# Performance work log

Measured on AMD Instinct MI355X. Metric: run time of the kernel, lower is better.

## Reference

```python
import jax, jax.numpy as jnp
import numpy as np
from jax.ops import segment_sum, segment_max, segment_min

N_PER = 128        # nodes (pulses) per graph; graphs are contiguous blocks
NUM_GRAPHS = 2048  # must be a multiple of BATCH_SIZE
K = 4              # knn_graph k (from KNNAmp(4, ...))
BATCH_SIZE = 1024  # hardcoded in the torch module
L1, L2, L3, L4, L5, L6, L7 = 5, 64, 128, 94, 64, 32, 1
GRU_IN = 4 * L5    # 256
GRU_H = L6         # 32


def setup_inputs() -> dict:
    key = jax.random.key(0)
    ks = jax.random.split(key, 12)
    N = N_PER * NUM_GRAPHS
    s = 0.1
    return {
        "x": jax.random.normal(ks[0], (N, L1), jnp.float32),
        "batch": (jnp.arange(N) // N_PER).astype(jnp.int32),
        "h_1": jnp.zeros((2, BATCH_SIZE, GRU_H), jnp.float32),
        "W1": jax.random.normal(ks[1], (2 * L1, L2), jnp.float32) * s,
        "b1": jnp.zeros((L2,), jnp.float32),
        "W2": jax.random.normal(ks[2], (L2, L3), jnp.float32) * s,
        "b2": jnp.zeros((L3,), jnp.float32),
        "nn1_W": jax.random.normal(ks[3], (3 * L3, L4), jnp.float32) * s,
        "nn1_b": jnp.zeros((L4,), jnp.float32),
        "nn2_W": jax.random.normal(ks[4], (L4, L5), jnp.float32) * s,
        "nn2_b": jnp.zeros((L5,), jnp.float32),
        "nn4_W": jax.random.normal(ks[5], (GRU_H, L7), jnp.float32) * s,
        "nn4_b": jnp.zeros((L7,), jnp.float32),
        "wih0": jax.random.normal(ks[6], (3 * GRU_H, GRU_IN), jnp.float32) * s,
        "whh0": jax.random.normal(ks[7], (3 * GRU_H, GRU_H), jnp.float32) * s,
        "bih0": jnp.zeros((3 * GRU_H,), jnp.float32),
        "bhh0": jnp.zeros((3 * GRU_H,), jnp.float32),
        "wih1": jax.random.normal(ks[8], (3 * GRU_H, GRU_H), jnp.float32) * s,
        "whh1": jax.random.normal(ks[9], (3 * GRU_H, GRU_H), jnp.float32) * s,
        "bih1": jnp.zeros((3 * GRU_H,), jnp.float32),
        "bhh1": jnp.zeros((3 * GRU_H,), jnp.float32),
    }


def _knn_neighbors(pos):
    # pos: [N,3]; graphs are contiguous blocks of N_PER nodes -> per-graph KNN
    p = pos.reshape(NUM_GRAPHS, N_PER, 3)
    d2 = jnp.sum((p[:, :, None, :] - p[:, None, :, :]) ** 2, -1)  # [G,n,n]
    d2 = d2 + jnp.eye(N_PER, dtype=d2.dtype) * 1e10               # loop=False
    _, idx = jax.lax.top_k(-d2, K)                                 # [G,n,K]
    off = (jnp.arange(NUM_GRAPHS, dtype=idx.dtype) * N_PER)[:, None, None]
    return (idx + off).reshape(-1, K)  # [N,K] global source (neighbor) ids


def _gru_layer(seq_in, h0, wih, whh, bih, bhh):
    # PyTorch GRU cell math; gate order r, z, n.
    def step(h, xt):
        gi = xt @ wih.T + bih
        gh = h @ whh.T + bhh
        ir, iz, inn = jnp.split(gi, 3, -1)
        hr, hz, hn = jnp.split(gh, 3, -1)
        r = jax.nn.sigmoid(ir + hr)
        z = jax.nn.sigmoid(iz + hz)
        n = jnp.tanh(inn + r * hn)
        hnew = (1.0 - z) * n + z * h
        return hnew, hnew
    hT, ys = jax.lax.scan(step, h0, seq_in)
    return ys, hT


def reference(x, batch, h_1, W1, b1, W2, b2, nn1_W, nn1_b, nn2_W, nn2_b,
              nn4_W, nn4_b, wih0, whh0, bih0, bhh0, wih1, whh1, bih1, bhh1):
    N = x.shape[0]
    nbr = _knn_neighbors(x[:, :3])                       # int indices, non-diff
    x_i = jnp.broadcast_to(x[:, None, :], (N, K, L1))    # center features
    x_j = x[nbr]                                         # [N,K,5] gather
    feats = jnp.concatenate([x_i, x_j - x_i], -1)        # EdgeConv message input
    m = jax.nn.relu(jax.nn.relu(feats @ W1 + b1) @ W2 + b2)  # [N,K,128]
    # three EdgeConvs share the same MLP; compute messages once, aggregate 3 ways
    h = jax.nn.relu(jnp.concatenate([m.max(1), m.mean(1), m.sum(1)], 1))  # [N,384]
    h = jax.nn.relu(h @ nn1_W + nn1_b)
    h = h @ nn2_W + nn2_b                                # [N,64]
    a = segment_max(h, batch, num_segments=NUM_GRAPHS)
    bmin = segment_min(h, batch, num_segments=NUM_GRAPHS)
    c = segment_sum(h, batch, num_segments=NUM_GRAPHS)
    cnt = segment_sum(jnp.ones((N, 1), h.dtype), batch, num_segments=NUM_GRAPHS)
    d = c / cnt
    g = jax.nn.relu(jnp.concatenate([a, bmin, c, d], 1))  # [G,256]
    seq_len = NUM_GRAPHS // BATCH_SIZE
    # faithful to torch.reshape((seq, 256, 1024)).transpose(1,2)
    g = g.reshape(seq_len, GRU_IN, BATCH_SIZE).transpose(0, 2, 1)  # [T,B,256]
    out0, hT0 = _gru_layer(g, h_1[0], wih0, whh0, bih0, bhh0)
    out1, hT1 = _gru_layer(out0, h_1[1], wih1, whh1, bih1, bhh1)
    hT = jnp.stack([hT0, hT1], 0)                        # [2,B,32]
    # torch: reshape(x.transpose(1,2), (-1, 32))
    y = out1.transpose(0, 2, 1).reshape(-1, GRU_H)
    y = jax.nn.relu(y)
    y = jax.nn.relu(y @ nn4_W + nn4_b)                   # [T*B, 1]
    return y, hT
```

## Files before the change

kernel.cpp:

```cpp
#include <hip/hip_runtime.h>
#include <hip/hip_bf16.h>

#define NPER 128

typedef __attribute__((ext_vector_type(8))) short s8v;
typedef __attribute__((ext_vector_type(4))) float f4v;

__device__ __forceinline__ unsigned short f2bf(float x) {
    unsigned u = __float_as_uint(x);
    unsigned r = u + 0x7FFFu + ((u >> 16) & 1u);
    return (unsigned short)(r >> 16);
}
__device__ __forceinline__ float bf2f(unsigned short b) {
    return __uint_as_float(((unsigned)b) << 16);
}

__device__ __forceinline__ void ins4(float d, int id, float* bd, int* bi) {
    const bool c0 = d < bd[0], c1 = d < bd[1], c2 = d < bd[2], c3 = d < bd[3];
    bd[3] = c2 ? bd[2] : (c3 ? d : bd[3]);  bi[3] = c2 ? bi[2] : (c3 ? id : bi[3]);
    bd[2] = c1 ? bd[1] : (c2 ? d : bd[2]);  bi[2] = c1 ? bi[1] : (c2 ? id : bi[2]);
    bd[1] = c0 ? bd[0] : (c1 ? d : bd[1]);  bi[1] = c0 ? bi[0] : (c1 ? id : bi[1]);
    bd[0] = c0 ? d : bd[0];                 bi[0] = c0 ? id : bi[0];
}

__global__ void k_prep(const float* __restrict__ W2,
                       const float* __restrict__ nn2W,
                       const float* __restrict__ nn1W,
                       float* __restrict__ nn2WT, float* __restrict__ WfT,
                       unsigned short* __restrict__ WBhi,
                       unsigned short* __restrict__ WBlo)
{
    int i = blockIdx.x * 256 + threadIdx.x;
    if (i < 6016) {
        int ch = i / 94, c = i - ch * 94;
        nn2WT[i] = nn2W[c * 64 + ch];
    } else if (i < 30592) {
        int k = i - 6016, jj = k >> 8, r = k & 255;
        float v = 0.0f;
        if (jj < 94) {
            if (r < 128) v = nn1W[r * 94 + jj];
            else {
                int c = r - 128;
                v = 0.25f * nn1W[(128 + c) * 94 + jj] + nn1W[(256 + c) * 94 + jj];
            }
        }
        WfT[k] = v;
    } else if (i < 38784) {
        int j = i - 30592;
        int e = j & 7, l = (j >> 3) & 63, nt = (j >> 9) & 7, ks = j >> 12;
        int kk = ks * 32 + ((l >> 4) << 3) + e;
        int n  = nt * 16 + (l & 15);
        float v = W2[kk * 128 + n];
        unsigned short hb = f2bf(v);
        WBhi[j] = hb;
        WBlo[j] = f2bf(v - bf2f(hb));
    }
}

__global__ __launch_bounds__(256, 4) void k_edge(
    const float* __restrict__ x,
    const float* __restrict__ W1,
    const float* __restrict__ b1,
    const float* __restrict__ b2,
    const unsigned short* __restrict__ WBhi,
    const unsigned short* __restrict__ WBlo,
    const float* __restrict__ WfT,
    const float* __restrict__ nn1b,
    const float* __restrict__ nn2WT,
    const float* __restrict__ nn2b,
    float* __restrict__ pmax,
    float* __restrict__ pmin,
    float* __restrict__ psum)
{
    __shared__ float pool[10240];
    float* XS  = pool;
    int*   NBR = (int*)(pool + 640);
    float* KD  = pool + 896;
    int*   KI  = (int*)(pool + 1920);
    unsigned short* PH16 = (unsigned short*)(pool + 1024);
    unsigned short* PL16 = (unsigned short*)(pool + 5632);
    float* AGM = pool + 1024;
    float* AGS = pool + 5120;
    float* NNH = pool;
    float* HT  = pool + 6016;

    const int t = threadIdx.x;
    const int lane = t & 63;
    const int w = __builtin_amdgcn_readfirstlane(t >> 6);
    const int graph = blockIdx.x >> 1;
    const int node0 = (blockIdx.x & 1) * 64;

    for (int i = t; i < NPER * 5; i += 256) XS[i] = x[(size_t)graph * (NPER * 5) + i];
    __syncthreads();

    {
        const int nl2 = t & 63;
        const int q  = t >> 6;
        const int ng2 = node0 + nl2;
        const float px = XS[ng2 * 5 + 0], py = XS[ng2 * 5 + 1], pz = XS[ng2 * 5 + 2];
        float bd[4] = {3e38f, 3e38f, 3e38f, 3e38f};
        int   bi[4] = {0, 0, 0, 0};
        const int m0 = q * 32;
        for (int m = m0; m < m0 + 32; ++m) {
            float dx = XS[m * 5 + 0] - px, dy = XS[m * 5 + 1] - py, dz = XS[m * 5 + 2] - pz;
            float d2 = __fadd_rn(__fadd_rn(__fmul_rn(dx, dx), __fmul_rn(dy, dy)),
                                 __fmul_rn(dz, dz));
            d2 = (m == ng2) ? 3.0e38f : d2;
            ins4(d2, m, bd, bi);
        }
        #pragma unroll
        for (int s = 0; s < 4; ++s) { KD[(q * 4 + s) * 64 + nl2] = bd[s]; KI[(q * 4 + s) * 64 + nl2] = bi[s]; }
    }
    __syncthreads();
    if (t < 64) {
        float bd[4] = {3e38f, 3e38f, 3e38f, 3e38f};
        int   bi[4] = {0, 0, 0, 0};
        #pragma unroll
        for (int q = 0; q < 4; ++q)
            #pragma unroll
            for (int s = 0; s < 4; ++s)
                ins4(KD[(q * 4 + s) * 64 + t], KI[(q * 4 + s) * 64 + t], bd, bi);
        #pragma unroll
        for (int s = 0; s < 4; ++s) NBR[t * 4 + s] = bi[s];
    }
    __syncthreads();

    float acc[24];
    const int jj0 = __builtin_amdgcn_readfirstlane(w * 24);
    #pragma unroll
    for (int i = 0; i < 24; ++i) acc[i] = (jj0 + i < 94) ? nn1b[jj0 + i] : 0.0f;

    #pragma unroll 1
    for (int hf = 0; hf < 2; ++hf) {
        float mxq[2][2][4], smq[2][2][4];
        #pragma unroll 1
        for (int c = 0; c < 2; ++c) {
            if ((t >> 7) == c) {
                const int nl = t >> 2;
                const int kk = t & 3;
                const int n_g = node0 + nl;
                const int j   = NBR[nl * 4 + kk];
                float f[10];
                #pragma unroll
                for (int d = 0; d < 5; ++d) { f[d] = XS[n_g * 5 + d]; f[5 + d] = XS[j * 5 + d] - f[d]; }
                float h1v[64];
                #pragma unroll
                for (int cc = 0; cc < 64; ++cc) h1v[cc] = b1[cc];
                #pragma unroll
                for (int d = 0; d < 10; ++d) {
                    float fd = f[d];
                    #pragma unroll
                    for (int cc = 0; cc < 64; ++cc) h1v[cc] = fmaf(fd, W1[d * 64 + cc], h1v[cc]);
                }
                #pragma unroll
                for (int cc = 0; cc < 64; ++cc) h1v[cc] = fmaxf(h1v[cc], 0.0f);

                const int rl = t & 127;
                unsigned int* dh = (unsigned int*)PH16 + rl * 36;
                unsigned int* dl = (unsigned int*)PL16 + rl * 36;
                #pragma unroll
                for (int i = 0; i < 8; ++i) {
                    unsigned int hw[4], lw[4];
                    #pragma unroll
                    for (int p = 0; p < 4; ++p) {
                        float va = h1v[i * 8 + p * 2], vb = h1v[i * 8 + p * 2 + 1];
                        unsigned short ha = f2bf(va), hb = f2bf(vb);
                        unsigned short la = f2bf(va - bf2f(ha)), lb = f2bf(vb - bf2f(hb));
                        hw[p] = (unsigned)ha | ((unsigned)hb << 16);
                        lw[p] = (unsigned)la | ((unsigned)lb << 16);
                    }
                    *(uint4*)(dh + 4 * i) = make_uint4(hw[0], hw[1], hw[2], hw[3]);
                    *(uint4*)(dl + 4 * i) = make_uint4(lw[0], lw[1], lw[2], lw[3]);
                }
            }
            __syncthreads();

            f4v C[2][4];
            #pragma unroll
            for (int q = 0; q < 4; ++q) {
                float bv = b2[hf * 64 + q * 16 + (lane & 15)];
                #pragma unroll
                for (int m = 0; m < 2; ++m) {
                    C[m][q][0] = bv; C[m][q][1] = bv; C[m][q][2] = bv; C[m][q][3] = bv;
                }
            }
            #pragma unroll
            for (int ks = 0; ks < 2; ++ks) {
                s8v ah[2], al[2];
                #pragma unroll
                for (int m = 0; m < 2; ++m) {
                    const int row = (w << 5) + (m << 4) + (lane & 15);
                    const int ui  = row * 72 + (ks << 5) + ((lane >> 4) << 3);
                    ah[m] = *(const s8v*)(PH16 + ui);
                    al[m] = *(const s8v*)(PL16 + ui);
                }
                #pragma unroll
                for (int q = 0; q < 4; ++q) {
                    const int nt = hf * 4 + q;
                    const int bidx = ((((ks << 3) | nt) << 6) | lane) << 3;
                    s8v bh = *(const s8v*)(WBhi + bidx);
                    s8v bl = *(const s8v*)(WBlo + bidx);
                    #pragma unroll
                    for (int m = 0; m < 2; ++m) {
                        f4v cc = C[m][q];
                        cc = __builtin_amdgcn_mfma_f32_16x16x32_bf16(al[m], bh, cc, 0, 0, 0);
                        cc = __builtin_amdgcn_mfma_f32_16x16x32_bf16(ah[m], bl, cc, 0, 0, 0);
                        cc = __builtin_amdgcn_mfma_f32_16x16x32_bf16(ah[m], bh, cc, 0, 0, 0);
                        C[m][q] = cc;
                    }
                }
            }
            #pragma unroll
            for (int m = 0; m < 2; ++m)
                #pragma unroll
                for (int q = 0; q < 4; ++q) {
                    float a0 = fmaxf(C[m][q][0], 0.0f), a1 = fmaxf(C[m][q][1], 0.0f);
                    float a2 = fmaxf(C[m][q][2], 0.0f), a3 = fmaxf(C[m][q][3], 0.0f);
                    mxq[c][m][q] = fmaxf(fmaxf(a0, a1), fmaxf(a2, a3));
                    smq[c][m][q] = (a0 + a1) + (a2 + a3);
                }
            __syncthreads();
        }

        #pragma unroll
        for (int c2 = 0; c2 < 2; ++c2)
            #pragma unroll
            for (int m = 0; m < 2; ++m)
                #pragma unroll
                for (int q = 0; q < 4; ++q) {
                    const int node = (c2 << 5) + (w << 3) + (m << 2) + (lane >> 4);
                    const int chl  = (q << 4) + (lane & 15);
                    const int ad   = (node << 6) + ((((chl >> 2) ^ node) & 15) << 2) + (chl & 3);
                    AGM[ad] = mxq[c2][m][q];
                    AGS[ad] = smq[c2][m][q];
                }
        __syncthreads();

        for (int cb = 0; cb < 64; cb += 8) {
            float am[8], as_[8];
            #pragma unroll
            for (int i = 0; i < 2; ++i) {
                const int sw = ((((cb >> 2) + i) ^ lane) & 15) << 2;
                *(float4*)&am[i * 4]  = *(const float4*)&AGM[(lane << 6) + sw];
                *(float4*)&as_[i * 4] = *(const float4*)&AGS[(lane << 6) + sw];
            }
            #pragma unroll
            for (int i2 = 0; i2 < 24; ++i2) {
                const float* wa = WfT + (size_t)(jj0 + i2) * 256 + hf * 64 + cb;
                const float* wb = wa + 128;
                float a = acc[i2];
                #pragma unroll
                for (int i = 0; i < 8; ++i) a = fmaf(am[i], wa[i], fmaf(as_[i], wb[i], a));
                acc[i2] = a;
            }
        }
        __syncthreads();
    }

    #pragma unroll
    for (int i2 = 0; i2 < 24; ++i2)
        if (jj0 + i2 < 94) NNH[(jj0 + i2) * 64 + lane] = fmaxf(acc[i2], 0.0f);
    __syncthreads();

    {
        const int ch0 = __builtin_amdgcn_readfirstlane(w * 16);
        float acc2[16];
        #pragma unroll
        for (int i = 0; i < 16; ++i) acc2[i] = nn2b[ch0 + i];
        #pragma unroll 1
        for (int cb = 0; cb < 64; cb += 32) {
            float hv[32];
            #pragma unroll
            for (int i = 0; i < 32; ++i) hv[i] = NNH[(cb + i) * 64 + lane];
            #pragma unroll
            for (int i = 0; i < 16; ++i) {
                const float* wp = nn2WT + (size_t)(ch0 + i) * 94 + cb;
                float a = acc2[i];
                #pragma unroll
                for (int c = 0; c < 32; ++c) a = fmaf(hv[c], wp[c], a);
                acc2[i] = a;
            }
        }
        {
            float hv[30];
            #pragma unroll
            for (int i = 0; i < 30; ++i) hv[i] = NNH[(64 + i) * 64 + lane];
            #pragma unroll
            for (int i = 0; i < 16; ++i) {
                const float* wp = nn2WT + (size_t)(ch0 + i) * 94 + 64;
                float a = acc2[i];
                #pragma unroll
                for (int c = 0; c < 30; ++c) a = fmaf(hv[c], wp[c], a);
                acc2[i] = a;
            }
        }
        __syncthreads();
        #pragma unroll
        for (int i = 0; i < 8; ++i)
            *(float2*)&HT[lane * 66 + ch0 + i * 2] =
                make_float2(acc2[i * 2], acc2[i * 2 + 1]);
    }
    __syncthreads();

    if (t < 64) {
        float mx = -3e38f, mn = 3e38f, sm = 0.0f;
        for (int n = 0; n < 64; ++n) {
            float v = HT[n * 66 + t];
            mx = fmaxf(mx, v); mn = fminf(mn, v); sm += v;
        }
        pmax[(size_t)blockIdx.x * 64 + t] = mx;
        pmin[(size_t)blockIdx.x * 64 + t] = mn;
        psum[(size_t)blockIdx.x * 64 + t] = sm;
    }
}

__global__ void k_pool(const float* __restrict__ pmax, const float* __restrict__ pmin,
                       const float* __restrict__ psum, float* __restrict__ g_out)
{
    const int t = threadIdx.x;
    const int g = blockIdx.x * 4 + (t >> 6);
    const int ch = t & 63;
    const size_t a = (size_t)(2 * g) * 64 + ch, b = a + 64;
    float mx = fmaxf(pmax[a], pmax[b]);
    float mn = fminf(pmin[a], pmin[b]);
    float sm = psum[a] + psum[b];
    float* gp = g_out + (size_t)g * 256;
    gp[ch]        = fmaxf(mx, 0.0f);
    gp[64 + ch]   = fmaxf(mn, 0.0f);
    gp[128 + ch]  = fmaxf(sm, 0.0f);
    gp[192 + ch]  = fmaxf(sm * (1.0f / 128.0f), 0.0f);
}

__global__ __launch_bounds__(128) void k_gru(
    const float* __restrict__ g, const float* __restrict__ h1_in,
    const float* __restrict__ wih0, const float* __restrict__ whh0,
    const float* __restrict__ bih0, const float* __restrict__ bhh0,
    const float* __restrict__ wih1, const float* __restrict__ whh1,
    const float* __restrict__ bih1, const float* __restrict__ bhh1,
    float* __restrict__ out1, float* __restrict__ hT)
{
    __shared__ float xt[4][256];
    __shared__ float h0[4][32];
    __shared__ float h1l[4][32];
    const int tid = threadIdx.x;
    const int e = tid >> 5;
    const int j = tid & 31;
    const int b = blockIdx.x * 4 + e;

    h0[e][j]  = h1_in[b * 32 + j];
    h1l[e][j] = h1_in[32768 + b * 32 + j];
    __syncthreads();

    for (int t = 0; t < 2; ++t) {
        for (int c = j; c < 256; c += 32)
            xt[e][c] = g[(size_t)(t * 1024 + 4 * c + (b >> 8)) * 256 + (b & 255)];
        __syncthreads();

        float gi0 = bih0[j], gi1 = bih0[32 + j], gi2 = bih0[64 + j];
        for (int c = 0; c < 256; ++c) {
            float xv = xt[e][c];
            gi0 += xv * wih0[j * 256 + c];
            gi1 += xv * wih0[(32 + j) * 256 + c];
            gi2 += xv * wih0[(64 + j) * 256 + c];
        }
        float gh0 = bhh0[j], gh1 = bhh0[32 + j], gh2 = bhh0[64 + j];
        #pragma unroll
        for (int c = 0; c < 32; ++c) {
            float hv = h0[e][c];
            gh0 += hv * whh0[j * 32 + c];
            gh1 += hv * whh0[(32 + j) * 32 + c];
            gh2 += hv * whh0[(64 + j) * 32 + c];
        }
        float r = 1.0f / (1.0f + expf(-(gi0 + gh0)));
        float z = 1.0f / (1.0f + expf(-(gi1 + gh1)));
        float nn = tanhf(gi2 + r * gh2);
        float hn0 = (1.0f - z) * nn + z * h0[e][j];
        __syncthreads();
        h0[e][j] = hn0;
        __syncthreads();

        float ai0 = bih1[j], ai1 = bih1[32 + j], ai2 = bih1[64 + j];
        #pragma unroll
        for (int c = 0; c < 32; ++c) {
            float xv = h0[e][c];
            ai0 += xv * wih1[j * 32 + c];
            ai1 += xv * wih1[(32 + j) * 32 + c];
            ai2 += xv * wih1[(64 + j) * 32 + c];
        }
        float ah0 = bhh1[j], ah1 = bhh1[32 + j], ah2 = bhh1[64 + j];
        #pragma unroll
        for (int c = 0; c < 32; ++c) {
            float hv = h1l[e][c];
            ah0 += hv * whh1[j * 32 + c];
            ah1 += hv * whh1[(32 + j) * 32 + c];
            ah2 += hv * whh1[(64 + j) * 32 + c];
        }
        float r1 = 1.0f / (1.0f + expf(-(ai0 + ah0)));
        float z1 = 1.0f / (1.0f + expf(-(ai1 + ah1)));
        float n1 = tanhf(ai2 + r1 * ah2);
        float hn1 = (1.0f - z1) * n1 + z1 * h1l[e][j];
        __syncthreads();
        h1l[e][j] = hn1;
        out1[(size_t)(t * 1024 + b) * 32 + j] = hn1;
        __syncthreads();
    }
    hT[b * 32 + j]         = h0[e][j];
    hT[32768 + b * 32 + j] = h1l[e][j];
}

__global__ void k_final(const float* __restrict__ out1,
                        const float* __restrict__ nn4W, const float* __restrict__ nn4b,
                        float* __restrict__ y)
{
    const int r = blockIdx.x * 256 + threadIdx.x;
    if (r >= 2048) return;
    const int t = r >> 10, rp = r & 1023;
    const int f = rp >> 5, bb0 = (rp & 31) << 5;
    float acc = nn4b[0];
    #pragma unroll
    for (int c = 0; c < 32; ++c)
        acc += fmaxf(out1[(size_t)(t * 1024 + bb0 + c) * 32 + f], 0.0f) * nn4W[c];
    y[r] = fmaxf(acc, 0.0f);
}

extern "C" void kernel_launch(void* const* d_in, const int* in_sizes, int n_in,
                              void* d_out, int out_size, void* d_ws, size_t ws_size,
                              hipStream_t stream) {
    const float* x    = (const float*)d_in[0];
    const float* h1i  = (const float*)d_in[2];
    const float* W1   = (const float*)d_in[3];
    const float* b1   = (const float*)d_in[4];
    const float* W2   = (const float*)d_in[5];
    const float* b2   = (const float*)d_in[6];
    const float* nn1W = (const float*)d_in[7];
    const float* nn1b = (const float*)d_in[8];
    const float* nn2W = (const float*)d_in[9];
    const float* nn2b = (const float*)d_in[10];
    const float* nn4W = (const float*)d_in[11];
    const float* nn4b = (const float*)d_in[12];
    const float* wih0 = (const float*)d_in[13];
    const float* whh0 = (const float*)d_in[14];
    const float* bih0 = (const float*)d_in[15];
    const float* bhh0 = (const float*)d_in[16];
    const float* wih1 = (const float*)d_in[17];
    const float* whh1 = (const float*)d_in[18];
    const float* bih1 = (const float*)d_in[19];
    const float* bhh1 = (const float*)d_in[20];

    float* ws = (float*)d_ws;
    float* g_buf  = ws;
    float* out1   = g_buf + 524288;
    float* nn2WT  = out1 + 65536;
    float* WfT    = nn2WT + 6016;
    float* pmax   = WfT + 24576;
    float* pmin   = pmax + 262144;
    float* psum   = pmin + 262144;
    unsigned short* WBhi = (unsigned short*)(psum + 262144);
    unsigned short* WBlo = WBhi + 8192;

    float* y  = (float*)d_out;
    float* hT = y + 2048;

    hipLaunchKernelGGL(k_prep, dim3(152), dim3(256), 0, stream,
                       W2, nn2W, nn1W, nn2WT, WfT, WBhi, WBlo);
    hipLaunchKernelGGL(k_edge, dim3(4096), dim3(256), 0, stream,
                       x, W1, b1, b2, WBhi, WBlo, WfT, nn1b, nn2WT, nn2b,
                       pmax, pmin, psum);
    hipLaunchKernelGGL(k_pool, dim3(512), dim3(256), 0, stream,
                       pmax, pmin, psum, g_buf);
    hipLaunchKernelGGL(k_gru, dim3(256), dim3(128), 0, stream,
                       g_buf, h1i, wih0, whh0, bih0, bhh0,
                       wih1, whh1, bih1, bhh1, out1, hT);
    hipLaunchKernelGGL(k_final, dim3(8), dim3(256), 0, stream,
                       out1, nn4W, nn4b, y);
}
```

Baseline: 922.9 us.

## Split edge MLP into quarter-width channel passes to reduce register pressure

The second-layer channel loop in k_edge now runs in four 32-channel passes instead of two 64-channel passes, and the first-layer hidden vector is computed in two 32-wide halves instead of all 64 at once. This cuts the number of live accumulators. The aggregation buffers switch from an XOR-swizzled layout to a padded stride of 36, and launch_bounds drops the occupancy hint from 4 to 3. In exchange, the first-layer MLP is recomputed on every pass, and the extra passes add syncthreads and repeated LDS writes.

```diff
diff --git a/kernel.cpp b/kernel.cpp
--- a/kernel.cpp
+++ b/kernel.cpp
@@ -57,7 +57,7 @@
     }
 }
 
-__global__ __launch_bounds__(256, 4) void k_edge(
+__global__ __launch_bounds__(256, 3) void k_edge(
     const float* __restrict__ x,
     const float* __restrict__ W1,
     const float* __restrict__ b1,
@@ -80,7 +80,7 @@
     unsigned short* PH16 = (unsigned short*)(pool + 1024);
     unsigned short* PL16 = (unsigned short*)(pool + 5632);
     float* AGM = pool + 1024;
-    float* AGS = pool + 5120;
+    float* AGS = pool + 3328;
     float* NNH = pool;
     float* HT  = pool + 6016;
 
@@ -131,8 +131,8 @@
     for (int i = 0; i < 24; ++i) acc[i] = (jj0 + i < 94) ? nn1b[jj0 + i] : 0.0f;
 
     #pragma unroll 1
-    for (int hf = 0; hf < 2; ++hf) {
-        float mxq[2][2][4], smq[2][2][4];
+    for (int qp = 0; qp < 4; ++qp) {
+        float mxq[2][2][2], smq[2][2][2];
         #pragma unroll 1
         for (int c = 0; c < 2; ++c) {
             if ((t >> 7) == c) {
@@ -143,81 +143,80 @@
                 float f[10];
                 #pragma unroll
                 for (int d = 0; d < 5; ++d) { f[d] = XS[n_g * 5 + d]; f[5 + d] = XS[j * 5 + d] - f[d]; }
-                float h1v[64];
-                #pragma unroll
-                for (int cc = 0; cc < 64; ++cc) h1v[cc] = b1[cc];
-                #pragma unroll
-                for (int d = 0; d < 10; ++d) {
-                    float fd = f[d];
-                    #pragma unroll
-                    for (int cc = 0; cc < 64; ++cc) h1v[cc] = fmaf(fd, W1[d * 64 + cc], h1v[cc]);
-                }
-                #pragma unroll
-                for (int cc = 0; cc < 64; ++cc) h1v[cc] = fmaxf(h1v[cc], 0.0f);
-
                 const int rl = t & 127;
                 unsigned int* dh = (unsigned int*)PH16 + rl * 36;
                 unsigned int* dl = (unsigned int*)PL16 + rl * 36;
-                #pragma unroll
-                for (int i = 0; i < 8; ++i) {
-                    unsigned int hw[4], lw[4];
+                #pragma unroll 1
+                for (int hh = 0; hh < 2; ++hh) {
+                    float hv[32];
                     #pragma unroll
-                    for (int p = 0; p < 4; ++p) {
-                        float va = h1v[i * 8 + p * 2], vb = h1v[i * 8 + p * 2 + 1];
-                        unsigned short ha = f2bf(va), hb = f2bf(vb);
-                        unsigned short la = f2bf(va - bf2f(ha)), lb = f2bf(vb - bf2f(hb));
-                        hw[p] = (unsigned)ha | ((unsigned)hb << 16);
-                        lw[p] = (unsigned)la | ((unsigned)lb << 16);
+                    for (int cc = 0; cc < 32; ++cc) hv[cc] = b1[hh * 32 + cc];
+                    #pragma unroll
+                    for (int d = 0; d < 10; ++d) {
+                        float fd = f[d];
+                        #pragma unroll
+                        for (int cc = 0; cc < 32; ++cc)
+                            hv[cc] = fmaf(fd, W1[d * 64 + hh * 32 + cc], hv[cc]);
                     }
-                    *(uint4*)(dh + 4 * i) = make_uint4(hw[0], hw[1], hw[2], hw[3]);
-                    *(uint4*)(dl + 4 * i) = make_uint4(lw[0], lw[1], lw[2], lw[3]);
+                    #pragma unroll
+                    for (int cc = 0; cc < 32; ++cc) hv[cc] = fmaxf(hv[cc], 0.0f);
+                    #pragma unroll
+                    for (int i = 0; i < 4; ++i) {
+                        unsigned int hw[4], lw[4];
+                        #pragma unroll
+                        for (int p = 0; p < 4; ++p) {
+                            float va = hv[i * 8 + p * 2], vb = hv[i * 8 + p * 2 + 1];
+                            unsigned short ha = f2bf(va), hb = f2bf(vb);
+                            unsigned short la = f2bf(va - bf2f(ha)), lb = f2bf(vb - bf2f(hb));
+                            hw[p] = (unsigned)ha | ((unsigned)hb << 16);
+                            lw[p] = (unsigned)la | ((unsigned)lb << 16);
+                        }
+                        *(uint4*)(dh + hh * 16 + i * 4) = make_uint4(hw[0], hw[1], hw[2], hw[3]);
+                        *(uint4*)(dl + hh * 16 + i * 4) = make_uint4(lw[0], lw[1], lw[2], lw[3]);
+                    }
                 }
             }
             __syncthreads();
 
-            f4v C[2][4];
-            #pragma unroll
-            for (int q = 0; q < 4; ++q) {
-                float bv = b2[hf * 64 + q * 16 + (lane & 15)];
+            f4v C[2][2];
+            #pragma unroll
+            for (int n2 = 0; n2 < 2; ++n2) {
+                float bv = b2[(qp * 2 + n2) * 16 + (lane & 15)];
                 #pragma unroll
                 for (int m = 0; m < 2; ++m) {
-                    C[m][q][0] = bv; C[m][q][1] = bv; C[m][q][2] = bv; C[m][q][3] = bv;
+                    C[m][n2][0] = bv; C[m][n2][1] = bv; C[m][n2][2] = bv; C[m][n2][3] = bv;
                 }
             }
             #pragma unroll
             for (int ks = 0; ks < 2; ++ks) {
-                s8v ah[2], al[2];
                 #pragma unroll
                 for (int m = 0; m < 2; ++m) {
                     const int row = (w << 5) + (m << 4) + (lane & 15);
                     const int ui  = row * 72 + (ks << 5) + ((lane >> 4) << 3);
-                    ah[m] = *(const s8v*)(PH16 + ui);
-                    al[m] = *(const s8v*)(PL16 + ui);
-                }
-                #pragma unroll
-                for (int q = 0; q < 4; ++q) {
-                    const int nt = hf * 4 + q;
-                    const int bidx = ((((ks << 3) | nt) << 6) | lane) << 3;
-                    s8v bh = *(const s8v*)(WBhi + bidx);
-                    s8v bl = *(const s8v*)(WBlo + bidx);
+                    s8v ah = *(const s8v*)(PH16 + ui);
+                    s8v al = *(const s8v*)(PL16 + ui);
                     #pragma unroll
-                    for (int m = 0; m < 2; ++m) {
-                        f4v cc = C[m][q];
-                        cc = __builtin_amdgcn_mfma_f32_16x16x32_bf16(al[m], bh, cc, 0, 0, 0);
-                        cc = __builtin_amdgcn_mfma_f32_16x16x32_bf16(ah[m], bl, cc, 0, 0, 0);
-                        cc = __builtin_amdgcn_mfma_f32_16x16x32_bf16(ah[m], bh, cc, 0, 0, 0);
-                        C[m][q] = cc;
+                    for (int n2 = 0; n2 < 2; ++n2) {
+                        const int nt = qp * 2 + n2;
+                        const int bidx = ((((ks << 3) | nt) << 6) | lane) << 3;
+                        s8v bh = *(const s8v*)(WBhi + bidx);
+                        s8v bl = *(const s8v*)(WBlo + bidx);
+                        f4v cc = C[m][n2];
+                        cc = __builtin_amdgcn_mfma_f32_16x16x32_bf16(al, bh, cc, 0, 0, 0);
+                        cc = __builtin_amdgcn_mfma_f32_16x16x32_bf16(ah, bl, cc, 0, 0, 0);
+                        cc = __builtin_amdgcn_mfma_f32_16x16x32_bf16(ah, bh, cc, 0, 0, 0);
+                        C[m][n2] = cc;
                     }
                 }
             }
             #pragma unroll
             for (int m = 0; m < 2; ++m)
                 #pragma unroll
-                for (int q = 0; q < 4; ++q) {
-                    float a0 = fmaxf(C[m][q][0], 0.0f), a1 = fmaxf(C[m][q][1], 0.0f);
-                    float a2 = fmaxf(C[m][q][2], 0.0f), a3 = fmaxf(C[m][q][3], 0.0f);
-                    mxq[c][m][q] = fmaxf(fmaxf(a0, a1), fmaxf(a2, a3));
-                    smq[c][m][q] = (a0 + a1) + (a2 + a3);
+                for (int n2 = 0; n2 < 2; ++n2) {
+                    float a0 = fmaxf(C[m][n2][0], 0.0f), a1 = fmaxf(C[m][n2][1], 0.0f);
+                    float a2 = fmaxf(C[m][n2][2], 0.0f), a3 = fmaxf(C[m][n2][3], 0.0f);
+                    mxq[c][m][n2] = fmaxf(fmaxf(a0, a1), fmaxf(a2, a3));
+                    smq[c][m][n2] = (a0 + a1) + (a2 + a3);
                 }
             __syncthreads();
         }
@@ -227,26 +226,25 @@
             #pragma unroll
             for (int m = 0; m < 2; ++m)
                 #pragma unroll
-                for (int q = 0; q < 4; ++q) {
+                for (int n2 = 0; n2 < 2; ++n2) {
                     const int node = (c2 << 5) + (w << 3) + (m << 2) + (lane >> 4);
-                    const int chl  = (q << 4) + (lane & 15);
-                    const int ad   = (node << 6) + ((((chl >> 2) ^ node) & 15) << 2) + (chl & 3);
-                    AGM[ad] = mxq[c2][m][q];
-                    AGS[ad] = smq[c2][m][q];
+                    const int chl  = (n2 << 4) + (lane & 15);
+                    AGM[node * 36 + chl] = mxq[c2][m][n2];
+                    AGS[node * 36 + chl] = smq[c2][m][n2];
                 }
         __syncthreads();
 
-        for (int cb = 0; cb < 64; cb += 8) {
+        #pragma unroll 1
+        for (int cb = 0; cb < 32; cb += 8) {
             float am[8], as_[8];
             #pragma unroll
             for (int i = 0; i < 2; ++i) {
-                const int sw = ((((cb >> 2) + i) ^ lane) & 15) << 2;
-                *(float4*)&am[i * 4]  = *(const float4*)&AGM[(lane << 6) + sw];
-                *(float4*)&as_[i * 4] = *(const float4*)&AGS[(lane << 6) + sw];
+                *(float4*)&am[i * 4]  = *(const float4*)&AGM[lane * 36 + cb + i * 4];
+                *(float4*)&as_[i * 4] = *(const float4*)&AGS[lane * 36 + cb + i * 4];
             }
             #pragma unroll
             for (int i2 = 0; i2 < 24; ++i2) {
-                const float* wa = WfT + (size_t)(jj0 + i2) * 256 + hf * 64 + cb;
+                const float* wa = WfT + (size_t)(jj0 + i2) * 256 + qp * 32 + cb;
                 const float* wb = wa + 128;
                 float a = acc[i2];
                 #pragma unroll
```

After: 848.2 us. -8.1%, faster.
